# Optimization experiments

Measured on AMD Instinct MI355X. Metric: run time of the kernel, lower is better.

The kernel has to match this reference:

```python
import jax, jax.numpy as jnp
import numpy as np

TOP_K = 2

def setup_inputs() -> dict:
    key = jax.random.key(0)
    k0, k1, k2, k3 = jax.random.split(key, 4)
    B, S, H, I, E = 2, 2048, 1024, 1408, 8
    hidden_states = jax.random.normal(k0, (B, S, H), dtype=jnp.float32)
    router_weight = jax.random.normal(k1, (E, H), dtype=jnp.float32) * 0.02
    gate_up_proj = jax.random.normal(k2, (E, 2 * I, H), dtype=jnp.float32) * 0.02
    down_proj = jax.random.normal(k3, (E, H, I), dtype=jnp.float32) * 0.02
    return {
        "hidden_states": hidden_states,
        "router_weight": router_weight,
        "gate_up_proj": gate_up_proj,
        "down_proj": down_proj,
    }

def reference(hidden_states, router_weight, gate_up_proj, down_proj):
    B, S, H = hidden_states.shape
    E = router_weight.shape[0]
    x = hidden_states.reshape(-1, H)                       # [T, H]
    T = x.shape[0]
    # Router: logits -> float32 softmax -> top-k (matches torch: topk on probs)
    logits = x @ router_weight.T                           # [T, E]
    probs = jax.nn.softmax(logits.astype(jnp.float32), axis=-1)
    topw, topi = jax.lax.top_k(probs, TOP_K)               # [T, K]
    topw = topw.astype(x.dtype)
    # Per-token combine weights over experts (zero for non-selected experts).
    combine = jnp.zeros((T, E), dtype=x.dtype)
    combine = combine.at[jnp.arange(T)[:, None], topi].set(topw)  # [T, E]
    # Dense grouped expert compute (same math as gather-GEMM-scatter loop:
    # tokens not routed to expert e get combine weight 0).
    gu = jnp.einsum('th,eoh->teo', x, gate_up_proj)        # [T, E, 2I]
    g, u = jnp.split(gu, 2, axis=-1)                       # [T, E, I] each
    h = jax.nn.silu(g) * u                                 # [T, E, I]
    y = jnp.einsum('tei,ehi->teh', h, down_proj)           # [T, E, H]
    out = jnp.einsum('teh,te->th', y, combine)             # [T, H]
    return out.reshape(B, S, H)
```

## Files before the change

### kernel.cpp

```cpp
#include <hip/hip_runtime.h>
#include <math.h>

#define NTOK 4096
#define HDIM 1024
#define NEXP 8
#define IDIM 1408
#define TWO_I 2816
#define TK 64
#define ROWCAP 10240

#define RT_BLKS 1024
#define CVG_BLKS 2048
#define G1J 22
#define G1_BLKS (8 * G1J * 10)
#define CVD_BLKS 256

typedef _Float16 f16x8 __attribute__((ext_vector_type(8)));
typedef float f32x4 __attribute__((ext_vector_type(4)));

typedef __attribute__((address_space(1))) const unsigned int gu32;
typedef __attribute__((address_space(3))) unsigned int lu32;
__device__ __forceinline__ void async16(const void* g, void* l) {
  __builtin_amdgcn_global_load_lds((gu32*)g, (lu32*)l, 16, 0, 0);
}

__device__ __forceinline__ void seg_prefix(const int* __restrict__ counts, int* aof) {
  int o = 0; aof[0] = 0;
#pragma unroll
  for (int i = 0; i < 8; i++) { o += (counts[i] + 255) & ~255; aof[i + 1] = o; }
}

__device__ __forceinline__ void cvt8(const float4* __restrict__ s, uint4* __restrict__ d, size_t idx) {
  float4 a = s[idx * 2], b = s[idx * 2 + 1];
  union { _Float16 h[8]; uint4 u; } p;
  p.h[0] = (_Float16)a.x; p.h[1] = (_Float16)a.y; p.h[2] = (_Float16)a.z; p.h[3] = (_Float16)a.w;
  p.h[4] = (_Float16)b.x; p.h[5] = (_Float16)b.y; p.h[6] = (_Float16)b.z; p.h[7] = (_Float16)b.w;
  d[idx] = p.u;
}

#define NG8 (NEXP * TWO_I * HDIM / 8)
#define ND8 (NEXP * HDIM * IDIM / 8)

extern "C" __global__ void moe_rcv(const float* __restrict__ x,
                                   const float* __restrict__ rw,
                                   int* __restrict__ topi,
                                   float* __restrict__ topw,
                                   _Float16* __restrict__ xh,
                                   int* __restrict__ cnt_part,
                                   const float* __restrict__ gup,
                                   _Float16* __restrict__ guph) {
  if (blockIdx.x >= RT_BLKS) {
    size_t idx = (size_t)(blockIdx.x - RT_BLKS) * 256 + threadIdx.x;
    const float4* s = (const float4*)gup; uint4* d = (uint4*)guph;
    for (; idx < NG8; idx += (size_t)CVG_BLKS * 256) cvt8(s, d, idx);
    return;
  }
  __shared__ int c8[NEXP];
  if (threadIdx.x < NEXP) c8[threadIdx.x] = 0;
  __syncthreads();
  int w = threadIdx.x >> 6, lane = threadIdx.x & 63;
  int t = blockIdx.x * 4 + w;
  const float4* xp = (const float4*)(x + (size_t)t * HDIM);
  const float4* rp = (const float4*)rw;
  float acc[NEXP];
#pragma unroll
  for (int e = 0; e < NEXP; e++) acc[e] = 0.f;
#pragma unroll
  for (int i = 0; i < HDIM / 256; i++) {
    float4 xv = xp[i * 64 + lane];
    union { _Float16 h[4]; uint2 u; } pk;
    pk.h[0] = (_Float16)xv.x; pk.h[1] = (_Float16)xv.y;
    pk.h[2] = (_Float16)xv.z; pk.h[3] = (_Float16)xv.w;
    *(uint2*)(xh + (size_t)t * HDIM + i * 256 + lane * 4) = pk.u;
#pragma unroll
    for (int e = 0; e < NEXP; e++) {
      float4 rv = rp[e * 256 + i * 64 + lane];
      acc[e] += xv.x * rv.x + xv.y * rv.y + xv.z * rv.z + xv.w * rv.w;
    }
  }
#pragma unroll
  for (int e = 0; e < NEXP; e++) {
#pragma unroll
    for (int off = 32; off > 0; off >>= 1) acc[e] += __shfl_down(acc[e], off);
  }
  if (lane == 0) {
    float m = acc[0];
    for (int e = 1; e < NEXP; e++) m = fmaxf(m, acc[e]);
    float p[NEXP], s = 0.f;
    for (int e = 0; e < NEXP; e++) { p[e] = __expf(acc[e] - m); s += p[e]; }
    float inv = 1.f / s;
    int i0 = 0; float b0 = p[0];
    for (int e = 1; e < NEXP; e++) if (p[e] > b0) { b0 = p[e]; i0 = e; }
    int i1 = -1; float b1 = -1.f;
    for (int e = 0; e < NEXP; e++) if (e != i0 && p[e] > b1) { b1 = p[e]; i1 = e; }
    topi[t * 2] = i0; topi[t * 2 + 1] = i1;
    topw[t * 2] = b0 * inv; topw[t * 2 + 1] = b1 * inv;
    atomicAdd(&c8[i0], 1);
    atomicAdd(&c8[i1], 1);
  }
  __syncthreads();
  if (threadIdx.x < NEXP) cnt_part[threadIdx.x * 1024 + blockIdx.x] = c8[threadIdx.x];
}

extern "C" __global__ void moe_scatter(const int* __restrict__ topi, const float* __restrict__ topw,
                                       const int* __restrict__ cnt_part, int* __restrict__ counts,
                                       int* __restrict__ tok, float* __restrict__ wrow,
                                       int* __restrict__ rows) {
  __shared__ int part16[16 * NEXP];
  __shared__ int cnt[NEXP];
  __shared__ int base[NEXP];
  __shared__ int tot_l[NEXP];
  const int tid = threadIdx.x, blk = blockIdx.x;
  if (tid < 128) {
    int g = tid >> 3, e = tid & 7;
    const int4* p = (const int4*)(cnt_part + e * 1024 + g * 64);
    int s = 0;
#pragma unroll
    for (int b = 0; b < 16; b++) { int4 v = p[b]; s += v.x + v.y + v.z + v.w; }
    part16[g * NEXP + e] = s;
  }
  if (tid < NEXP) cnt[tid] = 0;
  __syncthreads();
  if (tid < NEXP) {
    int tot = 0, pre = 0;
#pragma unroll
    for (int b = 0; b < 16; b++) {
      int v = part16[b * NEXP + tid];
      tot += v;
      if (b < blk) pre += v;
    }
    tot_l[tid] = tot;
    base[tid] = pre;
  }
  __syncthreads();
  if (tid < NEXP) {
    int o = 0;
    for (int i = 0; i < tid; i++) o += (tot_l[i] + 255) & ~255;
    base[tid] += o;
    if (blk == 0) counts[tid] = tot_l[tid];
  }
  __syncthreads();
  int t = blk * 256 + tid;
  int e0 = topi[t * 2], e1 = topi[t * 2 + 1];
  int r0 = atomicAdd(&cnt[e0], 1);
  int r1 = atomicAdd(&cnt[e1], 1);
  int row0 = base[e0] + r0;
  int row1 = base[e1] + r1;
  tok[row0] = t; wrow[row0] = topw[t * 2];     rows[t * 2]     = row0;
  tok[row1] = t; wrow[row1] = topw[t * 2 + 1]; rows[t * 2 + 1] = row1;
}

#define WAITVM(n) asm volatile("s_waitcnt vmcnt(" #n ")" ::: "memory")
#define BAR() __builtin_amdgcn_s_barrier()
#define PRIO(x) __builtin_amdgcn_s_setprio(x)
#define LDV(off) (*(const f16x8*)((const char*)smem + (uint32_t)(off)))

#define STG2(bf, kt) { \
  _Pragma("unroll") for (int c_ = 0; c_ < 4; c_++) { \
    async16(pA2[c_] + (size_t)(kt) * TK, smem + (bf) * 16384 + c_ * 2048 + tid * 8); \
    async16(pB2[c_] + (size_t)(kt) * TK, smem + (bf) * 16384 + 8192 + c_ * 2048 + tid * 8); } }

#define K128_SETUP() \
  const int lane = tid & 63, wv = tid >> 6; \
  const int wm = wv >> 1, wn = wv & 1; \
  const int quad = lane >> 4, l15 = lane & 15; \
  const int srow8 = tid >> 3; \
  const int kc = ((tid & 7) ^ (srow8 & 7)) << 3; \
  const uint32_t c0 = (uint32_t)((quad * 16) ^ ((l15 & 7) << 4)); \
  const uint32_t c1 = c0 ^ 64; \
  const uint32_t sA_0 = (uint32_t)((wm * 64 + l15) * 128) + c0; \
  const uint32_t sA_1 = (uint32_t)((wm * 64 + l15) * 128) + c1; \
  const uint32_t sB_0 = 16384u + (uint32_t)((wn * 64 + l15) * 128) + c0; \
  const uint32_t sB_1 = 16384u + (uint32_t)((wn * 64 + l15) * 128) + c1; \
  f32x4 acc2[4][4]; \
  _Pragma("unroll") for (int m = 0; m < 4; m++) \
  _Pragma("unroll") for (int n = 0; n < 4; n++) acc2[m][n] = (f32x4){0.f, 0.f, 0.f, 0.f}; \
  f16x8 va2[4][2], vb2[4][2];

#define K128_LOOP(NIT) { \
  STG2(0, 0); STG2(1, 1); \
  WAITVM(8); BAR(); \
  _Pragma("unroll 1") \
  for (int kt = 0; kt < (NIT); ++kt) { \
    const uint32_t BO = (kt & 1) ? 32768u : 0u; \
    _Pragma("unroll") for (int m_ = 0; m_ < 4; m_++) { \
      va2[m_][0] = LDV(sA_0 + BO + m_ * 2048); \
      va2[m_][1] = LDV(sA_1 + BO + m_ * 2048); } \
    _Pragma("unroll") for (int n_ = 0; n_ < 4; n_++) { \
      vb2[n_][0] = LDV(sB_0 + BO + n_ * 2048); \
      vb2[n_][1] = LDV(sB_1 + BO + n_ * 2048); } \
    asm volatile("s_waitcnt lgkmcnt(0)" ::: "memory"); \
    BAR(); \
    if (kt + 2 < (NIT)) { STG2((kt & 1), kt + 2); } \
    PRIO(1); \
    _Pragma("unroll") for (int k_ = 0; k_ < 2; k_++) \
    _Pragma("unroll") for (int m_ = 0; m_ < 4; m_++) \
    _Pragma("unroll") for (int n_ = 0; n_ < 4; n_++) \
      acc2[m_][n_] = __builtin_amdgcn_mfma_f32_16x16x32_f16( \
          va2[m_][k_], vb2[n_][k_], acc2[m_][n_], 0, 0, 0); \
    PRIO(0); \
    if (kt + 2 < (NIT)) { WAITVM(8); } else { WAITVM(0); } \
    BAR(); \
  } }

extern "C" __global__ __launch_bounds__(256, 2) void moe_gemm1cd(
    const _Float16* __restrict__ xh, const _Float16* __restrict__ guph,
    const int* __restrict__ counts, const int* __restrict__ tok,
    _Float16* __restrict__ hbuf,
    const float* __restrict__ dp, _Float16* __restrict__ dph) {
  __shared__ __align__(128) _Float16 smem[32768];
  const int tid = threadIdx.x;
  const int fid = blockIdx.x;
  if (fid >= G1_BLKS) {
    size_t idx = (size_t)(fid - G1_BLKS) * 256 + tid;
    const float4* s = (const float4*)dp; uint4* d = (uint4*)dph;
    for (; idx < ND8; idx += (size_t)CVD_BLKS * 256) cvt8(s, d, idx);
    return;
  }
  int aof[9]; seg_prefix(counts, aof);
  const int g = fid & 7, t7 = fid >> 3;
  const int j = t7 / 10, r10 = t7 - j * 10;
  const int rb = g + 8 * r10;
  const int row0 = rb * 128;
  if (row0 >= aof[8]) return;
  int e = 0;
#pragma unroll
  for (int i = 0; i < 8; i++) if (row0 >= aof[i]) e = i;
  const int lim = aof[e] + counts[e];

  K128_SETUP();

  const _Float16* pA2[4]; const _Float16* pB2[4];
#pragma unroll
  for (int c = 0; c < 4; c++) {
    int rowi = row0 + c * 32 + srow8;
    int tv = tok[rowi];
    int tk = (rowi < lim) ? tv : 0;
    pA2[c] = xh + (size_t)tk * HDIM + kc;
  }
  const _Float16* eb = guph + (size_t)e * TWO_I * HDIM;
#pragma unroll
  for (int c = 0; c < 4; c++) {
    int brow = (c < 2) ? (j * 64 + c * 32 + srow8)
                       : (IDIM + j * 64 + (c - 2) * 32 + srow8);
    pB2[c] = eb + (size_t)brow * HDIM + kc;
  }

  K128_LOOP(HDIM / TK)

  if (wn == 1) {
#pragma unroll
    for (int mf = 0; mf < 4; mf++)
#pragma unroll
      for (int nf = 0; nf < 4; nf++)
#pragma unroll
        for (int r2 = 0; r2 < 4; r2++)
          smem[(wm * 64 + mf * 16 + quad * 4 + r2) * 66 + nf * 16 + l15] =
              (_Float16)acc2[mf][nf][r2];
  }
  __syncthreads();
  if (wn == 0) {
#pragma unroll
    for (int mf = 0; mf < 4; mf++) {
#pragma unroll
      for (int r2 = 0; r2 < 4; r2++) {
        const int rl = wm * 64 + mf * 16 + quad * 4 + r2;
        _Float16* orow = hbuf + (size_t)(row0 + rl) * IDIM + j * 64;
#pragma unroll
        for (int nf = 0; nf < 4; nf++) {
          float gg = acc2[mf][nf][r2];
          float uu = (float)smem[rl * 66 + nf * 16 + l15];
          float hh = gg / (1.f + __expf(-gg)) * uu;
          orow[nf * 16 + l15] = (_Float16)hh;
        }
      }
    }
  }
}

extern "C" __global__ __launch_bounds__(256, 2) void moe_gemm2(
    const _Float16* __restrict__ hbuf, const _Float16* __restrict__ dph,
    const int* __restrict__ counts, const float* __restrict__ wrow,
    _Float16* __restrict__ yh) {
  __shared__ __align__(128) _Float16 smem[32768];
  int aof[9]; seg_prefix(counts, aof);
  const int fid = blockIdx.x;
  const int g = fid & 7, t7 = fid >> 3;
  const int cb = t7 / 10, r10 = t7 - cb * 10;
  const int rb = g + 8 * r10;
  const int row0 = rb * 128;
  if (row0 >= aof[8]) return;
  int e = 0;
#pragma unroll
  for (int i = 0; i < 8; i++) if (row0 >= aof[i]) e = i;

  const int tid = threadIdx.x;
  K128_SETUP();

  const _Float16* pA2[4]; const _Float16* pB2[4];
  const _Float16* eb = dph + (size_t)e * HDIM * IDIM;
#pragma unroll
  for (int c = 0; c < 4; c++) {
    pA2[c] = hbuf + (size_t)(row0 + c * 32 + srow8) * IDIM + kc;
    pB2[c] = eb + (size_t)(cb * 128 + c * 32 + srow8) * IDIM + kc;
  }

  K128_LOOP(IDIM / TK)

#pragma unroll
  for (int mf = 0; mf < 4; mf++) {
#pragma unroll
    for (int r2 = 0; r2 < 4; r2++) {
      const int row = row0 + wm * 64 + mf * 16 + quad * 4 + r2;
      const float wgt = wrow[row];
      _Float16* orow = yh + (size_t)row * HDIM + cb * 128 + wn * 64;
#pragma unroll
      for (int nf = 0; nf < 4; nf++)
        orow[nf * 16 + l15] = (_Float16)(acc2[mf][nf][r2] * wgt);
    }
  }
}

extern "C" __global__ void moe_combine(const _Float16* __restrict__ yh,
                                       const int* __restrict__ rows,
                                       float* __restrict__ out) {
  int i = blockIdx.x * 256 + threadIdx.x;
  int t = i >> 7, c8 = i & 127;
  int rA = rows[t * 2], rB = rows[t * 2 + 1];
  union { uint4 u; _Float16 h[8]; } pa, pb;
  pa.u = ((const uint4*)(yh + (size_t)rA * HDIM))[c8];
  pb.u = ((const uint4*)(yh + (size_t)rB * HDIM))[c8];
  float4 o0, o1;
  o0.x = (float)pa.h[0] + (float)pb.h[0]; o0.y = (float)pa.h[1] + (float)pb.h[1];
  o0.z = (float)pa.h[2] + (float)pb.h[2]; o0.w = (float)pa.h[3] + (float)pb.h[3];
  o1.x = (float)pa.h[4] + (float)pb.h[4]; o1.y = (float)pa.h[5] + (float)pb.h[5];
  o1.z = (float)pa.h[6] + (float)pb.h[6]; o1.w = (float)pa.h[7] + (float)pb.h[7];
  ((float4*)out)[(size_t)i * 2] = o0;
  ((float4*)out)[(size_t)i * 2 + 1] = o1;
}

extern "C" void kernel_launch(void* const* d_in, const int* in_sizes, int n_in,
                              void* d_out, int out_size, void* d_ws, size_t ws_size,
                              hipStream_t stream) {
  const float* x   = (const float*)d_in[0];
  const float* rw  = (const float*)d_in[1];
  const float* gup = (const float*)d_in[2];
  const float* dp  = (const float*)d_in[3];
  float* out = (float*)d_out;

  char* ws = (char*)d_ws;
  int*   counts   = (int*)ws;
  int*   cnt_part = (int*)(ws + 64);
  int*   topi   = (int*)(ws + 32832);
  float* topw   = (float*)(ws + 65600);
  int*   tok    = (int*)(ws + 98368);
  float* wrow   = (float*)(ws + 139328);
  int*   rows   = (int*)(ws + 180288);
  _Float16* xh   = (_Float16*)(ws + 213056);
  _Float16* guph = (_Float16*)(ws + 8601664);
  _Float16* dph  = (_Float16*)(ws + 54739008);
  _Float16* hbuf = (_Float16*)(ws + 77807680);
  _Float16* yh   = (_Float16*)(ws + 8601664);

  moe_rcv<<<RT_BLKS + CVG_BLKS, 256, 0, stream>>>(x, rw, topi, topw, xh, cnt_part, gup, guph);
  moe_scatter<<<NTOK / 256, 256, 0, stream>>>(topi, topw, cnt_part, counts, tok, wrow, rows);
  moe_gemm1cd<<<G1_BLKS + CVD_BLKS, 256, 0, stream>>>(xh, guph, counts, tok, hbuf, dp, dph);
  moe_gemm2<<<8 * 8 * 10, 256, 0, stream>>>(hbuf, dph, counts, wrow, yh);
  moe_combine<<<NTOK * HDIM / 8 / 256, 256, 0, stream>>>(yh, rows, out);
}
```

Measured before the change: 347.6 us.

## Use 256-row, 512-thread tiles in expert GEMMs with split-K double-buffered B

```diff
diff --git a/kernel.cpp b/kernel.cpp
--- a/kernel.cpp
+++ b/kernel.cpp
@@ -7,12 +7,12 @@
 #define IDIM 1408
 #define TWO_I 2816
 #define TK 64
-#define ROWCAP 10240
+#define NRB 40
+#define ROWCAP (NRB * 256)
 
 #define RT_BLKS 1024
 #define CVG_BLKS 2048
-#define G1J 22
-#define G1_BLKS (8 * G1J * 10)
+#define G1_BLKS 880
 #define CVD_BLKS 256
 
 typedef _Float16 f16x8 __attribute__((ext_vector_type(8)));
@@ -155,55 +155,55 @@
 #define PRIO(x) __builtin_amdgcn_s_setprio(x)
 #define LDV(off) (*(const f16x8*)((const char*)smem + (uint32_t)(off)))
 
-#define STG2(bf, kt) { \
-  _Pragma("unroll") for (int c_ = 0; c_ < 4; c_++) { \
-    async16(pA2[c_] + (size_t)(kt) * TK, smem + (bf) * 16384 + c_ * 2048 + tid * 8); \
-    async16(pB2[c_] + (size_t)(kt) * TK, smem + (bf) * 16384 + 8192 + c_ * 2048 + tid * 8); } }
-
-#define K128_SETUP() \
+#define K2_SETUP() \
   const int lane = tid & 63, wv = tid >> 6; \
-  const int wm = wv >> 1, wn = wv & 1; \
+  const int wm = wv >> 1, wn = wv & 1;             \
   const int quad = lane >> 4, l15 = lane & 15; \
-  const int srow8 = tid >> 3; \
-  const int kc = ((tid & 7) ^ (srow8 & 7)) << 3; \
+  const int srow8 = tid >> 3;                       \
+  const int kc = ((tid & 7) ^ (srow8 & 7)) << 3;    \
   const uint32_t c0 = (uint32_t)((quad * 16) ^ ((l15 & 7) << 4)); \
   const uint32_t c1 = c0 ^ 64; \
   const uint32_t sA_0 = (uint32_t)((wm * 64 + l15) * 128) + c0; \
   const uint32_t sA_1 = (uint32_t)((wm * 64 + l15) * 128) + c1; \
-  const uint32_t sB_0 = 16384u + (uint32_t)((wn * 64 + l15) * 128) + c0; \
-  const uint32_t sB_1 = 16384u + (uint32_t)((wn * 64 + l15) * 128) + c1; \
+  const uint32_t sB_0 = 32768u + (uint32_t)((wn * 64 + l15) * 128) + c0; \
+  const uint32_t sB_1 = 32768u + (uint32_t)((wn * 64 + l15) * 128) + c1; \
   f32x4 acc2[4][4]; \
   _Pragma("unroll") for (int m = 0; m < 4; m++) \
   _Pragma("unroll") for (int n = 0; n < 4; n++) acc2[m][n] = (f32x4){0.f, 0.f, 0.f, 0.f}; \
-  f16x8 va2[4][2], vb2[4][2];
-
-#define K128_LOOP(NIT) { \
-  STG2(0, 0); STG2(1, 1); \
-  WAITVM(8); BAR(); \
+  f16x8 va2[4], vb2[4];
+
+#define STGA(kt) { _Pragma("unroll") for (int c_ = 0; c_ < 4; c_++) \
+  async16(pA2[c_] + (size_t)(kt) * TK, smem + c_ * 4096 + tid * 8); }
+#define STGB(kt, buf) { _Pragma("unroll") for (int c_ = 0; c_ < 2; c_++) \
+  async16(pB2[c_] + (size_t)(kt) * TK, smem + 16384 + (buf) * 8192 + c_ * 4096 + tid * 8); }
+
+#define K2_RDA(CS) { _Pragma("unroll") for (int m_ = 0; m_ < 4; m_++) va2[m_] = LDV((CS) + m_ * 2048); }
+#define K2_RDB(CS) { _Pragma("unroll") for (int n_ = 0; n_ < 4; n_++) vb2[n_] = LDV((CS) + n_ * 2048); }
+#define K2_MM() { _Pragma("unroll") for (int m_ = 0; m_ < 4; m_++) \
+  _Pragma("unroll") for (int n_ = 0; n_ < 4; n_++) \
+    acc2[m_][n_] = __builtin_amdgcn_mfma_f32_16x16x32_f16(va2[m_], vb2[n_], acc2[m_][n_], 0, 0, 0); }
+
+#define K2_LOOP(NIT) { \
+  STGA(0); STGB(0, 0); STGB(1, 1); \
+  WAITVM(2); BAR(); \
   _Pragma("unroll 1") \
   for (int kt = 0; kt < (NIT); ++kt) { \
-    const uint32_t BO = (kt & 1) ? 32768u : 0u; \
-    _Pragma("unroll") for (int m_ = 0; m_ < 4; m_++) { \
-      va2[m_][0] = LDV(sA_0 + BO + m_ * 2048); \
-      va2[m_][1] = LDV(sA_1 + BO + m_ * 2048); } \
-    _Pragma("unroll") for (int n_ = 0; n_ < 4; n_++) { \
-      vb2[n_][0] = LDV(sB_0 + BO + n_ * 2048); \
-      vb2[n_][1] = LDV(sB_1 + BO + n_ * 2048); } \
-    asm volatile("s_waitcnt lgkmcnt(0)" ::: "memory"); \
-    BAR(); \
-    if (kt + 2 < (NIT)) { STG2((kt & 1), kt + 2); } \
-    PRIO(1); \
-    _Pragma("unroll") for (int k_ = 0; k_ < 2; k_++) \
-    _Pragma("unroll") for (int m_ = 0; m_ < 4; m_++) \
-    _Pragma("unroll") for (int n_ = 0; n_ < 4; n_++) \
-      acc2[m_][n_] = __builtin_amdgcn_mfma_f32_16x16x32_f16( \
-          va2[m_][k_], vb2[n_][k_], acc2[m_][n_], 0, 0, 0); \
-    PRIO(0); \
-    if (kt + 2 < (NIT)) { WAITVM(8); } else { WAITVM(0); } \
+    const uint32_t bo = (uint32_t)(kt & 1) * 16384u; \
+    K2_RDA(sA_0); K2_RDB(sB_0 + bo); \
+    PRIO(1); K2_MM(); PRIO(0);                     \
+    K2_RDA(sA_1); K2_RDB(sB_1 + bo); \
+    asm volatile("s_waitcnt lgkmcnt(0)" ::: "memory");   \
+    __builtin_amdgcn_sched_barrier(0); \
+    BAR();                                          \
+    if (kt + 1 < (NIT)) STGA(kt + 1);               \
+    if (kt + 2 < (NIT)) STGB(kt + 2, (kt & 1)); \
+    PRIO(1); K2_MM(); PRIO(0); \
+    if (kt + 2 < (NIT)) { WAITVM(2); }              \
+    else if (kt + 1 < (NIT)) { WAITVM(0); } \
     BAR(); \
   } }
 
-extern "C" __global__ __launch_bounds__(256, 2) void moe_gemm1cd(
+extern "C" __global__ __launch_bounds__(512, 4) void moe_gemm1cd(
     const _Float16* __restrict__ xh, const _Float16* __restrict__ guph,
     const int* __restrict__ counts, const int* __restrict__ tok,
     _Float16* __restrict__ hbuf,
@@ -212,41 +212,37 @@
   const int tid = threadIdx.x;
   const int fid = blockIdx.x;
   if (fid >= G1_BLKS) {
-    size_t idx = (size_t)(fid - G1_BLKS) * 256 + tid;
+    size_t idx = (size_t)(fid - G1_BLKS) * 512 + tid;
     const float4* s = (const float4*)dp; uint4* d = (uint4*)dph;
-    for (; idx < ND8; idx += (size_t)CVD_BLKS * 256) cvt8(s, d, idx);
+    for (; idx < ND8; idx += (size_t)CVD_BLKS * 512) cvt8(s, d, idx);
     return;
   }
   int aof[9]; seg_prefix(counts, aof);
-  const int g = fid & 7, t7 = fid >> 3;
-  const int j = t7 / 10, r10 = t7 - j * 10;
-  const int rb = g + 8 * r10;
-  const int row0 = rb * 128;
+  const int g = fid & 7, idx = fid >> 3;
+  const int j = idx / 5, r = idx - j * 5;
+  const int rb = g + 8 * r;
+  const int row0 = rb * 256;
   if (row0 >= aof[8]) return;
   int e = 0;
 #pragma unroll
   for (int i = 0; i < 8; i++) if (row0 >= aof[i]) e = i;
   const int lim = aof[e] + counts[e];
 
-  K128_SETUP();
-
-  const _Float16* pA2[4]; const _Float16* pB2[4];
+  K2_SETUP();
+
+  const _Float16* pA2[4]; const _Float16* pB2[2];
 #pragma unroll
   for (int c = 0; c < 4; c++) {
-    int rowi = row0 + c * 32 + srow8;
+    int rowi = row0 + c * 64 + srow8;
     int tv = tok[rowi];
     int tk = (rowi < lim) ? tv : 0;
     pA2[c] = xh + (size_t)tk * HDIM + kc;
   }
   const _Float16* eb = guph + (size_t)e * TWO_I * HDIM;
-#pragma unroll
-  for (int c = 0; c < 4; c++) {
-    int brow = (c < 2) ? (j * 64 + c * 32 + srow8)
-                       : (IDIM + j * 64 + (c - 2) * 32 + srow8);
-    pB2[c] = eb + (size_t)brow * HDIM + kc;
-  }
-
-  K128_LOOP(HDIM / TK)
+  pB2[0] = eb + (size_t)(j * 64 + srow8) * HDIM + kc;
+  pB2[1] = eb + (size_t)(IDIM + j * 64 + srow8) * HDIM + kc;
+
+  K2_LOOP(HDIM / TK)
 
   if (wn == 1) {
 #pragma unroll
@@ -278,34 +274,34 @@
   }
 }
 
-extern "C" __global__ __launch_bounds__(256, 2) void moe_gemm2(
+extern "C" __global__ __launch_bounds__(512, 4) void moe_gemm2(
     const _Float16* __restrict__ hbuf, const _Float16* __restrict__ dph,
     const int* __restrict__ counts, const float* __restrict__ wrow,
     _Float16* __restrict__ yh) {
   __shared__ __align__(128) _Float16 smem[32768];
   int aof[9]; seg_prefix(counts, aof);
+  const int tid = threadIdx.x;
   const int fid = blockIdx.x;
-  const int g = fid & 7, t7 = fid >> 3;
-  const int cb = t7 / 10, r10 = t7 - cb * 10;
-  const int rb = g + 8 * r10;
-  const int row0 = rb * 128;
+  const int g = fid & 7, idx = fid >> 3;
+  const int cb = idx / 5, r = idx - cb * 5;
+  const int rb = g + 8 * r;
+  const int row0 = rb * 256;
   if (row0 >= aof[8]) return;
   int e = 0;
 #pragma unroll
   for (int i = 0; i < 8; i++) if (row0 >= aof[i]) e = i;
 
-  const int tid = threadIdx.x;
-  K128_SETUP();
-
-  const _Float16* pA2[4]; const _Float16* pB2[4];
+  K2_SETUP();
+
+  const _Float16* pA2[4]; const _Float16* pB2[2];
+#pragma unroll
+  for (int c = 0; c < 4; c++)
+    pA2[c] = hbuf + (size_t)(row0 + c * 64 + srow8) * IDIM + kc;
   const _Float16* eb = dph + (size_t)e * HDIM * IDIM;
-#pragma unroll
-  for (int c = 0; c < 4; c++) {
-    pA2[c] = hbuf + (size_t)(row0 + c * 32 + srow8) * IDIM + kc;
-    pB2[c] = eb + (size_t)(cb * 128 + c * 32 + srow8) * IDIM + kc;
-  }
-
-  K128_LOOP(IDIM / TK)
+  pB2[0] = eb + (size_t)(cb * 128 + srow8) * IDIM + kc;
+  pB2[1] = eb + (size_t)(cb * 128 + 64 + srow8) * IDIM + kc;
+
+  K2_LOOP(IDIM / TK)
 
 #pragma unroll
   for (int mf = 0; mf < 4; mf++) {
@@ -364,7 +360,7 @@
 
   moe_rcv<<<RT_BLKS + CVG_BLKS, 256, 0, stream>>>(x, rw, topi, topw, xh, cnt_part, gup, guph);
   moe_scatter<<<NTOK / 256, 256, 0, stream>>>(topi, topw, cnt_part, counts, tok, wrow, rows);
-  moe_gemm1cd<<<G1_BLKS + CVD_BLKS, 256, 0, stream>>>(xh, guph, counts, tok, hbuf, dp, dph);
-  moe_gemm2<<<8 * 8 * 10, 256, 0, stream>>>(hbuf, dph, counts, wrow, yh);
+  moe_gemm1cd<<<G1_BLKS + CVD_BLKS, 512, 0, stream>>>(xh, guph, counts, tok, hbuf, dp, dph);
+  moe_gemm2<<<8 * 8 * 5, 512, 0, stream>>>(hbuf, dph, counts, wrow, yh);
   moe_combine<<<NTOK * HDIM / 8 / 256, 256, 0, stream>>>(yh, rows, out);
 }
```

Result: faster. 325.4 us (-6.4%).
